# Optimization experiments

Hardware: AMD Instinct MI355X
Metric: run time of the kernel (lower is better)

The kernel has to match this reference:

```python
import jax, jax.numpy as jnp
import numpy as np
from jax import lax

DIM = 384
NUM_HEADS = 12
HEAD_DIM = DIM // NUM_HEADS
SCALE = HEAD_DIM ** -0.5


def setup_inputs() -> dict:
    key = jax.random.key(0)
    ks = jax.random.split(key, 7)
    B, H, W = 8, 32, 32
    s = 0.02
    return {
        "x": jax.random.normal(ks[0], (B, DIM, H, W), jnp.float32),
        "qkvo_w": jax.random.normal(ks[1], (4 * DIM, DIM, 1, 1), jnp.float32) * s,
        "qkvo_b": jax.random.normal(ks[2], (4 * DIM,), jnp.float32) * s,
        "lepe_w": jax.random.normal(ks[3], (DIM, 1, 5, 5), jnp.float32) * s,
        "lepe_b": jax.random.normal(ks[4], (DIM,), jnp.float32) * s,
        "proj_w": jax.random.normal(ks[5], (DIM, DIM, 1, 1), jnp.float32) * s,
        "proj_b": jax.random.normal(ks[6], (DIM,), jnp.float32) * s,
    }


def reference(x, qkvo_w, qkvo_b, lepe_w, lepe_b, proj_w, proj_b):
    B, C, H, W = x.shape
    n, d = NUM_HEADS, HEAD_DIM
    HW = H * W

    # fused 1x1 QKVO projection: [B, 4C, H, W]
    qkvo = jnp.einsum('oc,bchw->bohw', qkvo_w[:, :, 0, 0], x) + qkvo_b[:, None, None]
    qkv = qkvo[:, :3 * C]
    o = qkvo[:, 3 * C:]

    # depthwise 5x5 LePE on v channels
    v_ch = qkv[:, 2 * C:]
    lepe = lax.conv_general_dilated(
        v_ch, lepe_w, window_strides=(1, 1), padding='SAME',
        feature_group_count=C,
        dimension_numbers=('NCHW', 'OIHW', 'NCHW')) + lepe_b[:, None, None]

    # split heads: channels ordered (m n d) -> q,k,v each [B, n, HW, d]
    q, k, v = jnp.transpose(qkv.reshape(B, 3, n, d, HW), (1, 0, 2, 4, 3))

    attn = jax.nn.softmax(SCALE * jnp.einsum('bnqd,bnkd->bnqk', q, k), axis=-1)
    res = jnp.einsum('bnqk,bnkd->bnqd', attn, v)  # [B, n, HW, d]
    res = jnp.transpose(res, (0, 1, 3, 2)).reshape(B, C, H, W)

    res = res + lepe
    out = jnp.einsum('oc,bchw->bohw', proj_w[:, :, 0, 0], res * o) + proj_b[:, None, None]
    return out
```

## Files before the change

kernel.cpp:

```cpp
#include <hip/hip_runtime.h>

#define DIM   384
#define NH    12
#define HD    32
#define HWSZ  1024
#define BATCH 8
#define SCALE 0.17677669529663687f
#define EXP_K (SCALE * 1.4426950408889634f)

typedef __attribute__((ext_vector_type(8))) short bf16x8;
typedef __attribute__((ext_vector_type(4))) float floatx4;

__device__ __forceinline__ unsigned short f2bf(float f) {
    union { float f; unsigned int u; } v; v.f = f;
    unsigned int u = v.u;
    u += 0x7fffu + ((u >> 16) & 1u);
    return (unsigned short)(u >> 16);
}
__device__ __forceinline__ float bf2f(unsigned short h) {
    union { unsigned int u; float f; } v; v.u = ((unsigned int)h) << 16;
    return v.f;
}

__global__ __launch_bounds__(256) void tcast_f32(
    const float* __restrict__ in, unsigned short* __restrict__ out, int C, int N)
{
    __shared__ __align__(16) unsigned short t[32][36];
    const int n0 = blockIdx.x * 32, c0 = blockIdx.y * 32, b = blockIdx.z;
    const float* ib = in + (size_t)b * C * N;
    unsigned short* ob = out + (size_t)b * N * C;
    const int tid = threadIdx.x;
    const int r = tid >> 3, q = (tid & 7) * 4;
    float4 f = *(const float4*)&ib[(size_t)(c0 + r) * N + n0 + q];
    ushort4 h = make_ushort4(f2bf(f.x), f2bf(f.y), f2bf(f.z), f2bf(f.w));
    *(ushort4*)&t[r][q] = h;
    __syncthreads();
    ushort4 o;
    o.x = t[q + 0][r]; o.y = t[q + 1][r]; o.z = t[q + 2][r]; o.w = t[q + 3][r];
    *(ushort4*)&ob[(size_t)(n0 + r) * C + c0 + q] = o;
}

__global__ __launch_bounds__(256) void tcast_b16(
    const unsigned short* __restrict__ in, unsigned short* __restrict__ out, int C, int N)
{
    __shared__ __align__(16) unsigned short t[32][36];
    const int n0 = blockIdx.x * 32, c0 = blockIdx.y * 32, b = blockIdx.z;
    const unsigned short* ib = in + (size_t)b * C * N;
    unsigned short* ob = out + (size_t)b * N * C;
    const int tid = threadIdx.x;
    const int r = tid >> 3, q = (tid & 7) * 4;
    ushort4 h = *(const ushort4*)&ib[(size_t)(c0 + r) * N + n0 + q];
    *(ushort4*)&t[r][q] = h;
    __syncthreads();
    ushort4 o;
    o.x = t[q + 0][r]; o.y = t[q + 1][r]; o.z = t[q + 2][r]; o.w = t[q + 3][r];
    *(ushort4*)&ob[(size_t)(n0 + r) * C + c0 + q] = o;
}

template<int MODE>
__global__ __launch_bounds__(256) void gemm_mfma(
    const float* __restrict__ W, const unsigned short* __restrict__ Xt,
    const float* __restrict__ bias, unsigned short* __restrict__ qkT,
    unsigned short* __restrict__ vo, float* __restrict__ Yf,
    int M, int K, int N)
{
    __shared__ __align__(16) unsigned short As[64][40];
    __shared__ __align__(16) unsigned short Bs[64][40];

    const int b = blockIdx.z, m0 = blockIdx.y * 64, n0 = blockIdx.x * 64;
    const int tid = threadIdx.x;
    const int w = tid >> 6, lane = tid & 63;
    const int g = lane >> 4, c = lane & 15;

    const unsigned short* Xb = Xt + (size_t)b * N * K;

    floatx4 acc[4];
    #pragma unroll
    for (int nb = 0; nb < 4; ++nb) acc[nb] = (floatx4){0.f, 0.f, 0.f, 0.f};

    for (int k0 = 0; k0 < K; k0 += 32) {
        __syncthreads();
        {
            const int mr = tid >> 2, k8 = (tid & 3) * 8;
            const float* wp = &W[(size_t)(m0 + mr) * K + k0 + k8];
            float4 wa = *(const float4*)wp;
            float4 wb = *(const float4*)(wp + 4);
            bf16x8 av;
            av[0] = (short)f2bf(wa.x); av[1] = (short)f2bf(wa.y);
            av[2] = (short)f2bf(wa.z); av[3] = (short)f2bf(wa.w);
            av[4] = (short)f2bf(wb.x); av[5] = (short)f2bf(wb.y);
            av[6] = (short)f2bf(wb.z); av[7] = (short)f2bf(wb.w);
            *(bf16x8*)&As[mr][k8] = av;
            const int nr = tid >> 2;
            *(bf16x8*)&Bs[nr][k8] = *(const bf16x8*)&Xb[(size_t)(n0 + nr) * K + k0 + k8];
        }
        __syncthreads();

        bf16x8 af = *(const bf16x8*)&As[16 * w + c][8 * g];
        #pragma unroll
        for (int nb = 0; nb < 4; ++nb) {
            bf16x8 bf = *(const bf16x8*)&Bs[nb * 16 + c][8 * g];
            acc[nb] = __builtin_amdgcn_mfma_f32_16x16x32_bf16(af, bf, acc[nb], 0, 0, 0);
        }
    }

    const int mbase = m0 + 16 * w + 4 * g;
    float bi[4];
    #pragma unroll
    for (int r = 0; r < 4; ++r) bi[r] = bias[mbase + r];

    if (MODE == 0) {
        if (m0 < 768) {
            #pragma unroll
            for (int nb = 0; nb < 4; ++nb) {
                const int n = n0 + nb * 16 + c;
                ushort4 h;
                h.x = f2bf(acc[nb][0] + bi[0]);
                h.y = f2bf(acc[nb][1] + bi[1]);
                h.z = f2bf(acc[nb][2] + bi[2]);
                h.w = f2bf(acc[nb][3] + bi[3]);
                *(ushort4*)&qkT[((size_t)b * HWSZ + n) * 768 + mbase] = h;
            }
        } else {
            #pragma unroll
            for (int nb = 0; nb < 4; ++nb) {
                const int n = n0 + nb * 16 + c;
                #pragma unroll
                for (int r = 0; r < 4; ++r)
                    vo[((size_t)b * 768 + (mbase - 768 + r)) * HWSZ + n] =
                        f2bf(acc[nb][r] + bi[r]);
            }
        }
    } else {
        #pragma unroll
        for (int nb = 0; nb < 4; ++nb) {
            const int n = n0 + nb * 16 + c;
            #pragma unroll
            for (int r = 0; r < 4; ++r)
                Yf[((size_t)b * M + mbase + r) * (size_t)N + n] = acc[nb][r] + bi[r];
        }
    }
}

__global__ __launch_bounds__(256) void attn_mfma(
    const unsigned short* __restrict__ qkT, const unsigned short* __restrict__ vo,
    unsigned short* __restrict__ res)
{
    __shared__ __align__(16) unsigned short Ks[64][40];
    __shared__ __align__(16) unsigned short Vs[32][72];
    __shared__ __align__(16) unsigned short Ps[64][72];
    __shared__ float lbuf[64];

    const int b = blockIdx.z, h = blockIdx.y, p0 = blockIdx.x * 64;
    const int tid = threadIdx.x;
    const int w = tid >> 6, lane = tid & 63;
    const int g = lane >> 4, c = lane & 15;

    const unsigned short* qkTb = qkT + (size_t)b * HWSZ * 768;
    const unsigned short* vb   = vo + ((size_t)b * 768 + h * HD) * HWSZ;

    bf16x8 qf = *(const bf16x8*)&qkTb[(size_t)(p0 + 16 * w + c) * 768 + h * HD + 8 * g];

    floatx4 oacc0 = (floatx4){0.f, 0.f, 0.f, 0.f};
    floatx4 oacc1 = (floatx4){0.f, 0.f, 0.f, 0.f};
    float Lacc = 0.f;

    for (int j0 = 0; j0 < HWSZ; j0 += 64) {
        __syncthreads();
        {
            const int jr = tid >> 2, d8 = (tid & 3) * 8;
            *(bf16x8*)&Ks[jr][d8] =
                *(const bf16x8*)&qkTb[(size_t)(j0 + jr) * 768 + 384 + h * HD + d8];
            const int dr = tid >> 3, j8 = (tid & 7) * 8;
            *(bf16x8*)&Vs[dr][j8] =
                *(const bf16x8*)&vb[(size_t)dr * HWSZ + j0 + j8];
        }
        __syncthreads();

        #pragma unroll
        for (int jb = 0; jb < 4; ++jb) {
            bf16x8 kf = *(const bf16x8*)&Ks[jb * 16 + c][8 * g];
            floatx4 st = (floatx4){0.f, 0.f, 0.f, 0.f};
            st = __builtin_amdgcn_mfma_f32_16x16x32_bf16(kf, qf, st, 0, 0, 0);
            float e0 = exp2f(st[0] * EXP_K);
            float e1 = exp2f(st[1] * EXP_K);
            float e2 = exp2f(st[2] * EXP_K);
            float e3 = exp2f(st[3] * EXP_K);
            Lacc += (e0 + e1) + (e2 + e3);
            ushort4 pe = make_ushort4(f2bf(e0), f2bf(e1), f2bf(e2), f2bf(e3));
            *(ushort4*)&Ps[16 * w + c][jb * 16 + 4 * g] = pe;
        }

        #pragma unroll
        for (int jk = 0; jk < 2; ++jk) {
            bf16x8 pf  = *(const bf16x8*)&Ps[16 * w + c][jk * 32 + 8 * g];
            bf16x8 vf0 = *(const bf16x8*)&Vs[c][jk * 32 + 8 * g];
            bf16x8 vf1 = *(const bf16x8*)&Vs[16 + c][jk * 32 + 8 * g];
            oacc0 = __builtin_amdgcn_mfma_f32_16x16x32_bf16(pf, vf0, oacc0, 0, 0, 0);
            oacc1 = __builtin_amdgcn_mfma_f32_16x16x32_bf16(pf, vf1, oacc1, 0, 0, 0);
        }
    }

    Lacc += __shfl_xor(Lacc, 16, 64);
    Lacc += __shfl_xor(Lacc, 32, 64);
    if (g == 0) lbuf[16 * w + c] = Lacc;

    float linv[4];
    #pragma unroll
    for (int r = 0; r < 4; ++r) linv[r] = 1.0f / lbuf[16 * w + 4 * g + r];

    unsigned short* rp = res + ((size_t)b * DIM + h * HD) * HWSZ;
    const int pbase = p0 + 16 * w + 4 * g;
    ushort4 h0, h1;
    h0.x = f2bf(oacc0[0] * linv[0]); h0.y = f2bf(oacc0[1] * linv[1]);
    h0.z = f2bf(oacc0[2] * linv[2]); h0.w = f2bf(oacc0[3] * linv[3]);
    h1.x = f2bf(oacc1[0] * linv[0]); h1.y = f2bf(oacc1[1] * linv[1]);
    h1.z = f2bf(oacc1[2] * linv[2]); h1.w = f2bf(oacc1[3] * linv[3]);
    *(ushort4*)&rp[(size_t)c * HWSZ + pbase] = h0;
    *(ushort4*)&rp[(size_t)(16 + c) * HWSZ + pbase] = h1;
}

__global__ __launch_bounds__(256) void lepe_mul(
    const unsigned short* __restrict__ vo, const float* __restrict__ lw,
    const float* __restrict__ lb, const unsigned short* __restrict__ res,
    unsigned short* __restrict__ gated)
{
    const int cch = blockIdx.x, b = blockIdx.y;
    const unsigned short* v  = vo + ((size_t)b * 768 + cch) * HWSZ;
    const unsigned short* o  = vo + ((size_t)b * 768 + 384 + cch) * HWSZ;
    const unsigned short* rp = res + ((size_t)b * DIM + cch) * HWSZ;
    unsigned short* gp = gated + ((size_t)b * DIM + cch) * HWSZ;

    __shared__ float vs[1024];
    __shared__ float wgt[25];

    const int tid = threadIdx.x;
    {
        ushort4 hv = *(const ushort4*)&v[tid * 4];
        vs[tid * 4 + 0] = bf2f(hv.x); vs[tid * 4 + 1] = bf2f(hv.y);
        vs[tid * 4 + 2] = bf2f(hv.z); vs[tid * 4 + 3] = bf2f(hv.w);
    }
    if (tid < 25) wgt[tid] = lw[cch * 25 + tid];
    __syncthreads();

    const float bias = lb[cch];
    const int q0 = tid * 4;
    const int y  = q0 >> 5;
    const int x0 = q0 & 31;

    float acc[4] = {bias, bias, bias, bias};
    #pragma unroll
    for (int ky = 0; ky < 5; ++ky) {
        int iy = y + ky - 2;
        if ((unsigned)iy < 32u) {
            #pragma unroll
            for (int kx = 0; kx < 5; ++kx) {
                float wv = wgt[ky * 5 + kx];
                #pragma unroll
                for (int u = 0; u < 4; ++u) {
                    int ix = x0 + u + kx - 2;
                    if ((unsigned)ix < 32u) acc[u] += wv * vs[iy * 32 + ix];
                }
            }
        }
    }

    ushort4 rh = *(const ushort4*)&rp[q0];
    ushort4 oh = *(const ushort4*)&o[q0];
    ushort4 outv;
    outv.x = f2bf((bf2f(rh.x) + acc[0]) * bf2f(oh.x));
    outv.y = f2bf((bf2f(rh.y) + acc[1]) * bf2f(oh.y));
    outv.z = f2bf((bf2f(rh.z) + acc[2]) * bf2f(oh.z));
    outv.w = f2bf((bf2f(rh.w) + acc[3]) * bf2f(oh.w));
    *(ushort4*)&gp[q0] = outv;
}

extern "C" void kernel_launch(void* const* d_in, const int* in_sizes, int n_in,
                              void* d_out, int out_size, void* d_ws, size_t ws_size,
                              hipStream_t stream)
{
    const float* x      = (const float*)d_in[0];
    const float* qkvo_w = (const float*)d_in[1];
    const float* qkvo_b = (const float*)d_in[2];
    const float* lepe_w = (const float*)d_in[3];
    const float* lepe_b = (const float*)d_in[4];
    const float* proj_w = (const float*)d_in[5];
    const float* proj_b = (const float*)d_in[6];

    unsigned short* xt     = (unsigned short*)d_ws;
    unsigned short* qkT    = xt     + (size_t)BATCH * HWSZ * DIM;
    unsigned short* vo     = qkT    + (size_t)BATCH * HWSZ * 768;
    unsigned short* res    = vo     + (size_t)BATCH * 768 * HWSZ;
    unsigned short* gated  = res    + (size_t)BATCH * DIM * HWSZ;
    unsigned short* gatedT = gated  + (size_t)BATCH * DIM * HWSZ;

    tcast_f32<<<dim3(32, 12, BATCH), 256, 0, stream>>>(x, xt, DIM, HWSZ);

    gemm_mfma<0><<<dim3(16, 24, BATCH), 256, 0, stream>>>(
        qkvo_w, xt, qkvo_b, qkT, vo, nullptr, 4 * DIM, DIM, HWSZ);

    attn_mfma<<<dim3(16, NH, BATCH), 256, 0, stream>>>(qkT, vo, res);

    lepe_mul<<<dim3(DIM, BATCH), 256, 0, stream>>>(vo, lepe_w, lepe_b, res, gated);

    tcast_b16<<<dim3(32, 12, BATCH), 256, 0, stream>>>(gated, gatedT, DIM, HWSZ);

    gemm_mfma<1><<<dim3(16, 6, BATCH), 256, 0, stream>>>(
        proj_w, gatedT, proj_b, nullptr, nullptr, (float*)d_out, DIM, DIM, HWSZ);
}
```

Measured before the change: 187.9 us.

## Pre-cast weights to bf16, deepen GEMM K tile, fold softmax scale into Q, enlarge attention block

A new kernel casts the QKVO and projection weights to bf16 once per call, so the GEMMs no longer convert fp32 weights on every tile. The GEMM K-step doubles to 64, halving the number of barrier pairs. The softmax scale and log2e factor are folded into Q at the GEMM epilogue, removing a multiply per score in attention. Attention blocks grow to 512 threads covering 128 queries, so each K/V tile is shared by more queries and the K and V loads are split across thread halves. f2bf now uses the HIP intrinsic. This adds an extra launch, workspace use, and rounding of the scaled Q to bf16.

```diff
diff --git a/kernel.cpp b/kernel.cpp
--- a/kernel.cpp
+++ b/kernel.cpp
@@ -1,4 +1,5 @@
 #include <hip/hip_runtime.h>
+#include <hip/hip_bf16.h>
 
 #define DIM   384
 #define NH    12
@@ -11,15 +12,30 @@
 typedef __attribute__((ext_vector_type(8))) short bf16x8;
 typedef __attribute__((ext_vector_type(4))) float floatx4;
 
-__device__ __forceinline__ unsigned short f2bf(float f) {
-    union { float f; unsigned int u; } v; v.f = f;
-    unsigned int u = v.u;
-    u += 0x7fffu + ((u >> 16) & 1u);
-    return (unsigned short)(u >> 16);
+__device__ __forceinline__ unsigned short f2bf(float x) {
+    union { __hip_bfloat16 h; unsigned short u; } c;
+    c.h = __float2bfloat16(x);
+    return c.u;
 }
 __device__ __forceinline__ float bf2f(unsigned short h) {
     union { unsigned int u; float f; } v; v.u = ((unsigned int)h) << 16;
     return v.f;
+}
+
+__global__ __launch_bounds__(256) void cast_w(
+    const float* __restrict__ wa, const float* __restrict__ wb,
+    unsigned short* __restrict__ da, unsigned short* __restrict__ db, int na8)
+{
+    const int idx = blockIdx.x * 256 + threadIdx.x;
+    const float* src; unsigned short* dst; int i;
+    if (idx < na8) { src = wa; dst = da; i = idx; }
+    else           { src = wb; dst = db; i = idx - na8; }
+    float4 f0 = *(const float4*)&src[i * 8];
+    float4 f1 = *(const float4*)&src[i * 8 + 4];
+    ushort4 h0 = make_ushort4(f2bf(f0.x), f2bf(f0.y), f2bf(f0.z), f2bf(f0.w));
+    ushort4 h1 = make_ushort4(f2bf(f1.x), f2bf(f1.y), f2bf(f1.z), f2bf(f1.w));
+    *(ushort4*)&dst[i * 8] = h0;
+    *(ushort4*)&dst[i * 8 + 4] = h1;
 }
 
 __global__ __launch_bounds__(256) void tcast_f32(
@@ -59,13 +75,13 @@
 
 template<int MODE>
 __global__ __launch_bounds__(256) void gemm_mfma(
-    const float* __restrict__ W, const unsigned short* __restrict__ Xt,
+    const unsigned short* __restrict__ Wb16, const unsigned short* __restrict__ Xt,
     const float* __restrict__ bias, unsigned short* __restrict__ qkT,
     unsigned short* __restrict__ vo, float* __restrict__ Yf,
     int M, int K, int N)
 {
-    __shared__ __align__(16) unsigned short As[64][40];
-    __shared__ __align__(16) unsigned short Bs[64][40];
+    __shared__ __align__(16) unsigned short As[64][72];
+    __shared__ __align__(16) unsigned short Bs[64][72];
 
     const int b = blockIdx.z, m0 = blockIdx.y * 64, n0 = blockIdx.x * 64;
     const int tid = threadIdx.x;
@@ -78,29 +94,28 @@
     #pragma unroll
     for (int nb = 0; nb < 4; ++nb) acc[nb] = (floatx4){0.f, 0.f, 0.f, 0.f};
 
-    for (int k0 = 0; k0 < K; k0 += 32) {
+    const int row = tid >> 2, cq = (tid & 3) * 16;
+
+    for (int k0 = 0; k0 < K; k0 += 64) {
         __syncthreads();
         {
-            const int mr = tid >> 2, k8 = (tid & 3) * 8;
-            const float* wp = &W[(size_t)(m0 + mr) * K + k0 + k8];
-            float4 wa = *(const float4*)wp;
-            float4 wb = *(const float4*)(wp + 4);
-            bf16x8 av;
-            av[0] = (short)f2bf(wa.x); av[1] = (short)f2bf(wa.y);
-            av[2] = (short)f2bf(wa.z); av[3] = (short)f2bf(wa.w);
-            av[4] = (short)f2bf(wb.x); av[5] = (short)f2bf(wb.y);
-            av[6] = (short)f2bf(wb.z); av[7] = (short)f2bf(wb.w);
-            *(bf16x8*)&As[mr][k8] = av;
-            const int nr = tid >> 2;
-            *(bf16x8*)&Bs[nr][k8] = *(const bf16x8*)&Xb[(size_t)(n0 + nr) * K + k0 + k8];
+            const unsigned short* wp = &Wb16[(size_t)(m0 + row) * K + k0 + cq];
+            *(bf16x8*)&As[row][cq]     = *(const bf16x8*)wp;
+            *(bf16x8*)&As[row][cq + 8] = *(const bf16x8*)(wp + 8);
+            const unsigned short* xp = &Xb[(size_t)(n0 + row) * K + k0 + cq];
+            *(bf16x8*)&Bs[row][cq]     = *(const bf16x8*)xp;
+            *(bf16x8*)&Bs[row][cq + 8] = *(const bf16x8*)(xp + 8);
         }
         __syncthreads();
 
-        bf16x8 af = *(const bf16x8*)&As[16 * w + c][8 * g];
+        bf16x8 af0 = *(const bf16x8*)&As[16 * w + c][8 * g];
+        bf16x8 af1 = *(const bf16x8*)&As[16 * w + c][32 + 8 * g];
         #pragma unroll
         for (int nb = 0; nb < 4; ++nb) {
-            bf16x8 bf = *(const bf16x8*)&Bs[nb * 16 + c][8 * g];
-            acc[nb] = __builtin_amdgcn_mfma_f32_16x16x32_bf16(af, bf, acc[nb], 0, 0, 0);
+            bf16x8 bf0 = *(const bf16x8*)&Bs[nb * 16 + c][8 * g];
+            bf16x8 bf1 = *(const bf16x8*)&Bs[nb * 16 + c][32 + 8 * g];
+            acc[nb] = __builtin_amdgcn_mfma_f32_16x16x32_bf16(af0, bf0, acc[nb], 0, 0, 0);
+            acc[nb] = __builtin_amdgcn_mfma_f32_16x16x32_bf16(af1, bf1, acc[nb], 0, 0, 0);
         }
     }
 
@@ -111,14 +126,15 @@
 
     if (MODE == 0) {
         if (m0 < 768) {
+            const float qs = (m0 < 384) ? EXP_K : 1.0f;
             #pragma unroll
             for (int nb = 0; nb < 4; ++nb) {
                 const int n = n0 + nb * 16 + c;
                 ushort4 h;
-                h.x = f2bf(acc[nb][0] + bi[0]);
-                h.y = f2bf(acc[nb][1] + bi[1]);
-                h.z = f2bf(acc[nb][2] + bi[2]);
-                h.w = f2bf(acc[nb][3] + bi[3]);
+                h.x = f2bf((acc[nb][0] + bi[0]) * qs);
+                h.y = f2bf((acc[nb][1] + bi[1]) * qs);
+                h.z = f2bf((acc[nb][2] + bi[2]) * qs);
+                h.w = f2bf((acc[nb][3] + bi[3]) * qs);
                 *(ushort4*)&qkT[((size_t)b * HWSZ + n) * 768 + mbase] = h;
             }
         } else {
@@ -142,16 +158,16 @@
     }
 }
 
-__global__ __launch_bounds__(256) void attn_mfma(
+__global__ __launch_bounds__(512) void attn_mfma(
     const unsigned short* __restrict__ qkT, const unsigned short* __restrict__ vo,
     unsigned short* __restrict__ res)
 {
     __shared__ __align__(16) unsigned short Ks[64][40];
     __shared__ __align__(16) unsigned short Vs[32][72];
-    __shared__ __align__(16) unsigned short Ps[64][72];
-    __shared__ float lbuf[64];
-
-    const int b = blockIdx.z, h = blockIdx.y, p0 = blockIdx.x * 64;
+    __shared__ __align__(16) unsigned short Ps[128][72];
+    __shared__ float lbuf[128];
+
+    const int b = blockIdx.z, h = blockIdx.y, p0 = blockIdx.x * 128;
     const int tid = threadIdx.x;
     const int w = tid >> 6, lane = tid & 63;
     const int g = lane >> 4, c = lane & 15;
@@ -167,11 +183,13 @@
 
     for (int j0 = 0; j0 < HWSZ; j0 += 64) {
         __syncthreads();
-        {
+        if (tid < 256) {
             const int jr = tid >> 2, d8 = (tid & 3) * 8;
             *(bf16x8*)&Ks[jr][d8] =
                 *(const bf16x8*)&qkTb[(size_t)(j0 + jr) * 768 + 384 + h * HD + d8];
-            const int dr = tid >> 3, j8 = (tid & 7) * 8;
+        } else {
+            const int t = tid - 256;
+            const int dr = t >> 3, j8 = (t & 7) * 8;
             *(bf16x8*)&Vs[dr][j8] =
                 *(const bf16x8*)&vb[(size_t)dr * HWSZ + j0 + j8];
         }
@@ -182,10 +200,10 @@
             bf16x8 kf = *(const bf16x8*)&Ks[jb * 16 + c][8 * g];
             floatx4 st = (floatx4){0.f, 0.f, 0.f, 0.f};
             st = __builtin_amdgcn_mfma_f32_16x16x32_bf16(kf, qf, st, 0, 0, 0);
-            float e0 = exp2f(st[0] * EXP_K);
-            float e1 = exp2f(st[1] * EXP_K);
-            float e2 = exp2f(st[2] * EXP_K);
-            float e3 = exp2f(st[3] * EXP_K);
+            float e0 = exp2f(st[0]);
+            float e1 = exp2f(st[1]);
+            float e2 = exp2f(st[2]);
+            float e3 = exp2f(st[3]);
             Lacc += (e0 + e1) + (e2 + e3);
             ushort4 pe = make_ushort4(f2bf(e0), f2bf(e1), f2bf(e2), f2bf(e3));
             *(ushort4*)&Ps[16 * w + c][jb * 16 + 4 * g] = pe;
@@ -293,18 +311,23 @@
     unsigned short* res    = vo     + (size_t)BATCH * 768 * HWSZ;
     unsigned short* gated  = res    + (size_t)BATCH * DIM * HWSZ;
     unsigned short* gatedT = gated  + (size_t)BATCH * DIM * HWSZ;
+    unsigned short* wqb    = gatedT + (size_t)BATCH * HWSZ * DIM;
+    unsigned short* wpb    = wqb    + (size_t)1536 * DIM;
+
+    cast_w<<<dim3((73728 + 18432) / 256), 256, 0, stream>>>(
+        qkvo_w, proj_w, wqb, wpb, 73728);
 
     tcast_f32<<<dim3(32, 12, BATCH), 256, 0, stream>>>(x, xt, DIM, HWSZ);
 
     gemm_mfma<0><<<dim3(16, 24, BATCH), 256, 0, stream>>>(
-        qkvo_w, xt, qkvo_b, qkT, vo, nullptr, 4 * DIM, DIM, HWSZ);
-
-    attn_mfma<<<dim3(16, NH, BATCH), 256, 0, stream>>>(qkT, vo, res);
+        wqb, xt, qkvo_b, qkT, vo, nullptr, 4 * DIM, DIM, HWSZ);
+
+    attn_mfma<<<dim3(8, NH, BATCH), 512, 0, stream>>>(qkT, vo, res);
 
     lepe_mul<<<dim3(DIM, BATCH), 256, 0, stream>>>(vo, lepe_w, lepe_b, res, gated);
 
     tcast_b16<<<dim3(32, 12, BATCH), 256, 0, stream>>>(gated, gatedT, DIM, HWSZ);
 
     gemm_mfma<1><<<dim3(16, 6, BATCH), 256, 0, stream>>>(
-        proj_w, gatedT, proj_b, nullptr, nullptr, (float*)d_out, DIM, DIM, HWSZ);
-}
+        wpb, gatedT, proj_b, nullptr, nullptr, (float*)d_out, DIM, DIM, HWSZ);
+}
```

After: 173.0 us. 8.0% less time.
